# Kernel optimization log

Measured on AMD Instinct MI355X. Metric: run time of the kernel, lower is better.

Reference implementation:

```python
import jax, jax.numpy as jnp
from jax import lax
import numpy as np

B, C, PC, OC = 2, 256, 256, 256
H = W = 128
F = 2            # downsample_fac -> qkv conv kernel/stride and head upsample factor
NH, D = 4, C // 4  # 4 heads, attn_size = in_c//4
EPS = 1e-5


def conv2d(x, w, b, stride, padding):
    y = lax.conv_general_dilated(x, w, (stride, stride), padding,
                                 dimension_numbers=('NCHW', 'OIHW', 'NCHW'))
    return y + b[None, :, None, None]


def upsample_nearest(x, f):
    return jnp.repeat(jnp.repeat(x, f, axis=2), f, axis=3)


def setup_inputs() -> dict:
    key = jax.random.key(0)
    ks = jax.random.split(key, 16)
    s = 0.02  # small weight scale for numeric stability
    return {
        'app_enc':      jax.random.normal(ks[0], (B, C, H, W), jnp.float32),
        'app_pose_enc': jax.random.normal(ks[1], (B, C, H, W), jnp.float32),
        'pose_enc':     jax.random.normal(ks[2], (B, C, H, W), jnp.float32),
        'prev_inp':     jax.random.normal(ks[3], (B, PC, H // 2, W // 2), jnp.float32),
        'qw': jax.random.normal(ks[4], (NH, D, C, F, F), jnp.float32) * s,
        'qb': jax.random.normal(ks[5], (NH, D), jnp.float32) * s,
        'kw': jax.random.normal(ks[6], (NH, D, C, F, F), jnp.float32) * s,
        'kb': jax.random.normal(ks[7], (NH, D), jnp.float32) * s,
        'vw': jax.random.normal(ks[8], (NH, D, C, F, F), jnp.float32) * s,
        'vb': jax.random.normal(ks[9], (NH, D), jnp.float32) * s,
        'gamma': jax.random.normal(ks[10], (NH,), jnp.float32) * 0.1,
        'fw': jax.random.normal(ks[11], (C, 2 * C, 1, 1), jnp.float32) * s,
        'fb': jax.random.normal(ks[12], (C,), jnp.float32) * s,
        'cw': jax.random.normal(ks[13], (OC, C + PC, 3, 3), jnp.float32) * s,
        'cb': jax.random.normal(ks[14], (OC,), jnp.float32) * s,
    }


def reference(app_enc, app_pose_enc, pose_enc, prev_inp,
              qw, qb, kw, kb, vw, vb, gamma, fw, fb, cw, cb):
    # ---- AttnMech: 4 heads, q/k/v via stride-F convs over stacked heads ----
    def heads_proj(x, w, b):
        y = conv2d(x, w.reshape(NH * D, C, F, F), b.reshape(NH * D), F, 'VALID')
        _, _, h2, w2 = y.shape
        return y.reshape(B, NH, D, h2 * w2), h2, w2

    q, h2, w2 = heads_proj(pose_enc, qw, qb)        # [B,NH,D,N]
    k, _, _ = heads_proj(app_pose_enc, kw, kb)
    v, _, _ = heads_proj(app_enc, vw, vb)

    # unnormalized (no softmax) scaled dot-product attention, N = h2*w2
    attn = jnp.einsum('bhdn,bhdm->bhnm', q, k) / jnp.sqrt(jnp.float32(D))
    out = jnp.einsum('bhnm,bhdm->bhdn', attn, v)    # [B,NH,D,N]
    out = out.reshape(B, NH, D, h2, w2) * gamma[None, :, None, None, None]
    out = upsample_nearest(out.reshape(B, NH * D, h2, w2), F)  # back to [B,C,H,W]

    cat = jnp.concatenate([pose_enc, out], axis=1)  # [B, 2C, H, W]
    x = conv2d(cat, fw, fb, 1, 'VALID')             # 1x1 final_conv -> [B,C,H,W]

    # ---- GenDecAttnBlock tail: upsample prev, concat, ConvBlock ----
    prev = upsample_nearest(prev_inp, 2)            # [B,PC,H,W]
    x = jnp.concatenate([x, prev], axis=1)          # [B, C+PC, H, W]
    y = conv2d(x, cw, cb, 1, 'SAME')                # 3x3, pad 1
    mean = y.mean(axis=(2, 3), keepdims=True)
    var = y.var(axis=(2, 3), keepdims=True)         # biased, as torch InstanceNorm2d
    y = (y - mean) / jnp.sqrt(var + EPS)
    return jax.nn.relu(y)
```

## Files before the change

### kernel.cpp

```cpp
#include <hip/hip_runtime.h>
#include <hip/hip_bf16.h>

#define N2   4096
#define HWP  16384
#define EPSI 1e-5f

typedef unsigned short ushort_t;
typedef __attribute__((ext_vector_type(8))) short short8;
typedef __attribute__((ext_vector_type(4))) float f32x4;

static const size_t BUF0_OFF  = 0;
static const size_t BUF1_OFF  = 4194304;
static const size_t QT_OFF    = 8388608;
static const size_t KC_OFF    = 9437184;
static const size_t VC_OFF    = 10485760;
static const size_t S_OFF     = 11534336;
static const size_t SUM_OFF   = 11567104;
static const size_t SUM2_OFF  = 11567616;
static const size_t ZP_OFF    = 11568128;
static const size_t XCAT_OFF  = 11568192;
static const size_t PREVT_OFF = 15762496;
static const size_t WQ_OFF    = 16811072;
static const size_t WK_OFF    = 16942144;
static const size_t WV_OFF    = 17073216;
static const size_t WF_OFF    = 17204288;
static const size_t WA3X_OFF  = 17269824;
static const size_t WP_OFF    = 17564736;
static const size_t Y3_OFF    = BUF1_OFF;

__device__ __forceinline__ ushort_t f2bf(float x) {
    union { float f; unsigned u; } v; v.f = x;
    unsigned r = v.u + 0x7FFFu + ((v.u >> 16) & 1u);
    return (ushort_t)(r >> 16);
}
__device__ __forceinline__ float bf2f(ushort_t h) {
    union { unsigned u; float f; } v; v.u = ((unsigned)h) << 16; return v.f;
}
__device__ __forceinline__ void gload_lds16(const void* g, void* l) {
    __builtin_amdgcn_global_load_lds(
        (const __attribute__((address_space(1))) void*)g,
        (__attribute__((address_space(3))) void*)l, 16, 0, 0);
}

__global__ __launch_bounds__(256) void prep_k(const float* __restrict__ qw,
                                              const float* __restrict__ kw,
                                              const float* __restrict__ vw,
                                              const float* __restrict__ fw,
                                              const float* __restrict__ cw,
                                              const float* __restrict__ prev,
                                              float* __restrict__ wsf) {
    __shared__ ushort_t T[64][64];
    int sec = blockIdx.y, bx = blockIdx.x, t = threadIdx.x;
    if (sec < 3) {
        if (bx >= 256) return;
        int idx = bx * 256 + t;
        const float* src = sec == 0 ? qw : (sec == 1 ? kw : vw);
        ushort_t* dst = (ushort_t*)(wsf + (sec == 0 ? WQ_OFF : (sec == 1 ? WK_OFF : WV_OFF)));
        float4 v = *(const float4*)&src[(size_t)idx * 4];
        dst[0 * 65536 + idx] = f2bf(v.x);
        dst[1 * 65536 + idx] = f2bf(v.y);
        dst[2 * 65536 + idx] = f2bf(v.z);
        dst[3 * 65536 + idx] = f2bf(v.w);
    } else if (sec == 3) {
        int idx = bx * 256 + t;
        ((ushort_t*)(wsf + WF_OFF))[idx] = f2bf(fw[idx]);
    } else if (sec == 4) {
        int idx = bx * 256 + t;
        int oc = idx >> 9, c = idx & 511;
        const float* src = cw + (size_t)idx * 9;
        float w[9];
#pragma unroll
        for (int tp = 0; tp < 9; ++tp) w[tp] = src[tp];
        if (c < 256) {
            ushort_t* wA3x = (ushort_t*)(wsf + WA3X_OFF);
#pragma unroll
            for (int tp = 0; tp < 9; ++tp)
                wA3x[((size_t)tp * 256 + oc) * 256 + c] = f2bf(w[tp]);
        } else {
            int cc = c - 256;
            ushort_t* wP = (ushort_t*)(wsf + WP_OFF);
#pragma unroll
            for (int fx = 0; fx < 3; ++fx) {
                wP[((size_t)(0 * 6 + 0 * 3 + fx) * 256 + oc) * 256 + cc] = f2bf(w[fx]);
                wP[((size_t)(0 * 6 + 1 * 3 + fx) * 256 + oc) * 256 + cc] = f2bf(w[3 + fx] + w[6 + fx]);
                wP[((size_t)(1 * 6 + 0 * 3 + fx) * 256 + oc) * 256 + cc] = f2bf(w[fx] + w[3 + fx]);
                wP[((size_t)(1 * 6 + 1 * 3 + fx) * 256 + oc) * 256 + cc] = f2bf(w[6 + fx]);
            }
        }
    } else if (sec == 5) {
        int y2 = bx & 63, ct = (bx >> 6) & 3, b = bx >> 8;
        ushort_t* pT = (ushort_t*)(wsf + PREVT_OFF);
#pragma unroll
        for (int i = 0; i < 4; ++i) {
            int s = t + i * 256;
            int cc = s >> 4, xq = s & 15;
            float4 v = *(const float4*)&prev[(((size_t)b * 256 + ct * 64 + cc) * 64 + y2) * 64 + xq * 4];
            ushort4 h; h.x = f2bf(v.x); h.y = f2bf(v.y); h.z = f2bf(v.z); h.w = f2bf(v.w);
            *(ushort4*)&T[cc][xq * 4] = h;
        }
        __syncthreads();
#pragma unroll
        for (int i = 0; i < 2; ++i) {
            int w = t * 2 + i;
            int px = w >> 3, cbk = w & 7;
            short8 o;
#pragma unroll
            for (int j = 0; j < 8; ++j) o[j] = (short)T[cbk * 8 + j][px];
            *(short8*)&pT[((size_t)b * N2 + (size_t)y2 * 64 + px) * 256 + ct * 64 + cbk * 8] = o;
        }
    } else {
        int idx = bx * 256 + t;
        if (idx < 33856) wsf[S_OFF + idx] = 0.f;
    }
}

__device__ __forceinline__ void xpm_body(const float* __restrict__ in, ushort_t* __restrict__ xpm,
                                         int y, int ct, int b, int t) {
    __shared__ ushort_t T[64][128];
#pragma unroll
    for (int i = 0; i < 8; ++i) {
        int s = t + i * 256;
        int cc = s >> 5, xq = s & 31;
        float4 v = *(const float4*)&in[(((size_t)b * 256 + ct * 64 + cc) * 128 + y) * 128 + xq * 4];
        ushort4 h; h.x = f2bf(v.x); h.y = f2bf(v.y); h.z = f2bf(v.z); h.w = f2bf(v.w);
        *(ushort4*)&T[cc][xq * 4] = h;
    }
    __syncthreads();
#pragma unroll
    for (int i = 0; i < 4; ++i) {
        int w = t * 4 + i;
        int px = w >> 3, cbk = w & 7;
        short8 o;
#pragma unroll
        for (int j = 0; j < 8; ++j) o[j] = (short)T[cbk * 8 + j][px];
        *(short8*)&xpm[(((size_t)b * HWP) + (size_t)y * 128 + px) * 256 + ct * 64 + cbk * 8] = o;
    }
}

__global__ __launch_bounds__(256) void xpm2_k(const float* __restrict__ app,
                                              const float* __restrict__ app_pose,
                                              float* __restrict__ wsf) {
    int z = blockIdx.z, which = z >> 1, b = z & 1;
    const float* in = which == 0 ? app : app_pose;
    ushort_t* dst = (ushort_t*)(wsf + (which == 0 ? BUF0_OFF : BUF1_OFF));
    xpm_body(in, dst, blockIdx.x, blockIdx.y, b, threadIdx.x);
}

__global__ __launch_bounds__(256) void xpmP_k(const float* __restrict__ pose,
                                              float* __restrict__ wsf) {
    xpm_body(pose, (ushort_t*)(wsf + BUF0_OFF), blockIdx.x, blockIdx.y, blockIdx.z, threadIdx.x);
}

template<int MODE>
__device__ __forceinline__ void qkv_body(int nb, int oct, int b,
                                         const float* __restrict__ bias,
                                         const float* __restrict__ gamma,
                                         const ushort_t* __restrict__ wA,
                                         const ushort_t* __restrict__ xpm,
                                         ushort_t* __restrict__ outp) {
    int n0 = nb * 32, oc0 = oct * 128;
    __shared__ alignas(16) ushort_t As[2][128 * 64];
    __shared__ alignas(16) ushort_t Bs[2][32 * 64];
    int t = threadIdx.x, lane = t & 63, wv = t >> 6;
    int wm = wv >> 1, wn = wv & 1, l15 = lane & 15, lq = lane >> 4;
    f32x4 acc[4] = {};

    auto stage = [&](int chunk, int bufi) {
        int tap = chunk >> 2, c0 = (chunk & 3) << 6;
        int fy = tap >> 1, fx = tap & 1;
#pragma unroll
        for (int r = 0; r < 4; ++r) {
            int slot = t + r * 256;
            int row = slot >> 3, cbk = slot & 7;
            const ushort_t* src = wA + ((size_t)tap * 65536 + (size_t)(oc0 + row) * 256
                                        + c0 + ((cbk ^ (row & 7)) << 3));
            gload_lds16(src, (ushort_t*)As[bufi] + (((size_t)wv * 64 + r * 256) << 3));
        }
        {
            int n = t >> 3, cbk = t & 7;
            int ng = n0 + n;
            int iy = ((ng >> 6) << 1) + fy, ix = ((ng & 63) << 1) + fx;
            const ushort_t* src = xpm + (((size_t)b * HWP + (size_t)iy * 128 + ix) * 256
                                         + c0 + ((cbk ^ (n & 7)) << 3));
            gload_lds16(src, (ushort_t*)Bs[bufi] + ((size_t)wv * 64 << 3));
        }
    };

    stage(0, 0);
    __syncthreads();
    int buf = 0;
    for (int chunk = 0; chunk < 16; ++chunk) {
        short8 af[4][2], bf[2];
#pragma unroll
        for (int m = 0; m < 4; ++m) {
            int row = wm * 64 + m * 16 + l15;
#pragma unroll
            for (int ks = 0; ks < 2; ++ks)
                af[m][ks] = *(const short8*)&As[buf][row * 64 + (((ks * 4 + lq) ^ (row & 7)) << 3)];
        }
        {
            int col = wn * 16 + l15;
#pragma unroll
            for (int ks = 0; ks < 2; ++ks)
                bf[ks] = *(const short8*)&Bs[buf][col * 64 + (((ks * 4 + lq) ^ (col & 7)) << 3)];
        }
        if (chunk < 15) stage(chunk + 1, buf ^ 1);
#pragma unroll
        for (int ks = 0; ks < 2; ++ks)
#pragma unroll
            for (int m = 0; m < 4; ++m)
                acc[m] = __builtin_amdgcn_mfma_f32_16x16x32_bf16(af[m][ks], bf[ks], acc[m], 0, 0, 0);
        __syncthreads();
        buf ^= 1;
    }
#pragma unroll
    for (int m = 0; m < 4; ++m) {
        int col = wn * 16 + l15;
        int ng = n0 + col;
        int ocq = oc0 + wm * 64 + m * 16 + lq * 4;
        if (MODE == 0) {
            ushort4 o;
            float s0 = gamma[ocq >> 6] * 0.125f;
            o.x = f2bf((acc[m][0] + bias[ocq + 0]) * s0);
            o.y = f2bf((acc[m][1] + bias[ocq + 1]) * s0);
            o.z = f2bf((acc[m][2] + bias[ocq + 2]) * s0);
            o.w = f2bf((acc[m][3] + bias[ocq + 3]) * s0);
            *(ushort4*)&outp[((size_t)b * N2 + ng) * 256 + ocq] = o;
        } else {
#pragma unroll
            for (int r = 0; r < 4; ++r)
                outp[((size_t)(b * 256 + ocq + r)) * N2 + ng] = f2bf(acc[m][r] + bias[ocq + r]);
        }
    }
}

__global__ __launch_bounds__(256, 4) void kv_mfma(const float* __restrict__ kb_,
                                                  const float* __restrict__ vb_,
                                                  float* __restrict__ wsf) {
    int z = blockIdx.z, cv = z >> 1, b = z & 1;
    const ushort_t* wA  = (const ushort_t*)(wsf + (cv == 0 ? WV_OFF : WK_OFF));
    const ushort_t* xpm = (const ushort_t*)(wsf + (cv == 0 ? BUF0_OFF : BUF1_OFF));
    const float* bias   = cv == 0 ? vb_ : kb_;
    ushort_t* outp      = (ushort_t*)(wsf + (cv == 0 ? VC_OFF : KC_OFF));
    qkv_body<1>(blockIdx.x, blockIdx.y, b, bias, nullptr, wA, xpm, outp);
}

__global__ __launch_bounds__(256, 4) void q_mfma(const float* __restrict__ qb_,
                                                 const float* __restrict__ gamma,
                                                 float* __restrict__ wsf) {
    qkv_body<0>(blockIdx.x, blockIdx.y, blockIdx.z, qb_, gamma,
                (const ushort_t*)(wsf + WQ_OFF), (const ushort_t*)(wsf + BUF0_OFF),
                (ushort_t*)(wsf + QT_OFF));
}

__global__ __launch_bounds__(64) void attn_S_mfma(float* __restrict__ wsf) {
    int mc = blockIdx.x, bh = blockIdx.y;
    int b = bh >> 2, h = bh & 3;
    const ushort_t* vp = (const ushort_t*)(wsf + VC_OFF) + (size_t)(b * 256 + h * 64) * N2;
    const ushort_t* kp = (const ushort_t*)(wsf + KC_OFF) + (size_t)(b * 256 + h * 64) * N2;
    float* Sp = wsf + S_OFF + (size_t)bh * 4096;
    int lane = threadIdx.x, l15 = lane & 15, lq = lane >> 4;
    f32x4 acc[4][4] = {};
    for (int m0 = mc * 512; m0 < mc * 512 + 512; m0 += 32) {
        short8 af[4], bf[4];
#pragma unroll
        for (int mt = 0; mt < 4; ++mt)
            af[mt] = *(const short8*)&vp[(size_t)(mt * 16 + l15) * N2 + m0 + lq * 8];
#pragma unroll
        for (int nt = 0; nt < 4; ++nt)
            bf[nt] = *(const short8*)&kp[(size_t)(nt * 16 + l15) * N2 + m0 + lq * 8];
#pragma unroll
        for (int mt = 0; mt < 4; ++mt)
#pragma unroll
            for (int nt = 0; nt < 4; ++nt)
                acc[mt][nt] = __builtin_amdgcn_mfma_f32_16x16x32_bf16(
                    af[mt], bf[nt], acc[mt][nt], 0, 0, 0);
    }
#pragma unroll
    for (int mt = 0; mt < 4; ++mt)
#pragma unroll
        for (int nt = 0; nt < 4; ++nt)
#pragma unroll
            for (int r = 0; r < 4; ++r)
                atomicAdd(&Sp[(mt * 16 + lq * 4 + r) * 64 + nt * 16 + l15], acc[mt][nt][r]);
}

__global__ __launch_bounds__(256) void attn_O_mfma(float* __restrict__ wsf) {
    int nb = blockIdx.x, bh = blockIdx.y;
    int b = bh >> 2, h = bh & 3;
    const float* Sp = wsf + S_OFF + (size_t)bh * 4096;
    const ushort_t* qT = (const ushort_t*)(wsf + QT_OFF);
    ushort_t* attT = (ushort_t*)(wsf + KC_OFF);
    __shared__ ushort_t Sl[64][72];
    int t = threadIdx.x;
#pragma unroll
    for (int g = 0; g < 4; ++g) {
        int idx = t * 16 + g * 4;
        float4 v = *(const float4*)&Sp[idx];
        int row = idx >> 6, col = idx & 63;
        ushort4 o; o.x = f2bf(v.x); o.y = f2bf(v.y); o.z = f2bf(v.z); o.w = f2bf(v.w);
        *(ushort4*)&Sl[row][col] = o;
    }
    __syncthreads();
    int lane = t & 63, wv = t >> 6, l15 = lane & 15, lq = lane >> 4;
    int n_base = nb * 256 + wv * 64;
    f32x4 acc[4][4] = {};
#pragma unroll
    for (int ks = 0; ks < 2; ++ks) {
        short8 aS[4], bq[4];
#pragma unroll
        for (int mt = 0; mt < 4; ++mt)
            aS[mt] = *(const short8*)&Sl[mt * 16 + l15][ks * 32 + lq * 8];
#pragma unroll
        for (int nt = 0; nt < 4; ++nt)
            bq[nt] = *(const short8*)&qT[((size_t)b * N2 + n_base + nt * 16 + l15) * 256
                                         + h * 64 + ks * 32 + lq * 8];
#pragma unroll
        for (int mt = 0; mt < 4; ++mt)
#pragma unroll
            for (int nt = 0; nt < 4; ++nt)
                acc[mt][nt] = __builtin_amdgcn_mfma_f32_16x16x32_bf16(
                    aS[mt], bq[nt], acc[mt][nt], 0, 0, 0);
    }
#pragma unroll
    for (int mt = 0; mt < 4; ++mt)
#pragma unroll
        for (int nt = 0; nt < 4; ++nt) {
            int n = n_base + nt * 16 + l15;
            ushort4 o;
            o.x = f2bf(acc[mt][nt][0]); o.y = f2bf(acc[mt][nt][1]);
            o.z = f2bf(acc[mt][nt][2]); o.w = f2bf(acc[mt][nt][3]);
            *(ushort4*)&attT[((size_t)b * N2 + n) * 256 + h * 64 + mt * 16 + lq * 4] = o;
        }
}

__global__ __launch_bounds__(256, 3) void conv1x1_mfma(const float* __restrict__ fb,
                                                       float* __restrict__ wsf) {
    int lin = blockIdx.x;
    int swz = (lin & 7) * 128 + (lin >> 3);
    int xh = swz & 1, y = (swz >> 1) & 127, oct = (swz >> 8) & 1, b = swz >> 9;
    int oc0 = oct * 128, x0 = xh * 64;
    const ushort_t* wF   = (const ushort_t*)(wsf + WF_OFF);
    const ushort_t* xpm  = (const ushort_t*)(wsf + BUF0_OFF);
    const ushort_t* attT = (const ushort_t*)(wsf + KC_OFF);
    ushort_t* xcatT      = (ushort_t*)(wsf + XCAT_OFF);

    __shared__ alignas(16) ushort_t As[2][128 * 64];
    __shared__ alignas(16) ushort_t Bs[2][64 * 64];
    int t = threadIdx.x, lane = t & 63, wv = t >> 6;
    int wm = wv >> 1, wn = wv & 1, l15 = lane & 15, lq = lane >> 4;
    f32x4 acc[4][2] = {};

    auto stage = [&](int chunk, int bufi) {
        int c0 = chunk << 6;
#pragma unroll
        for (int r = 0; r < 4; ++r) {
            int slot = t + r * 256;
            int row = slot >> 3, cbk = slot & 7;
            const ushort_t* src = wF + ((size_t)(oc0 + row) * 512 + c0 + ((cbk ^ (row & 7)) << 3));
            gload_lds16(src, (ushort_t*)As[bufi] + (((size_t)wv * 64 + r * 256) << 3));
        }
#pragma unroll
        for (int r = 0; r < 2; ++r) {
            int slot = t + r * 256;
            int n = slot >> 3, cbk = slot & 7;
            int x = x0 + n;
            int sw = (cbk ^ (n & 7)) << 3;
            const ushort_t* src;
            if (c0 < 256)
                src = xpm + (((size_t)b * HWP + (size_t)y * 128 + x) * 256 + c0 + sw);
            else
                src = attT + (((size_t)b * N2 + (size_t)(y >> 1) * 64 + (x >> 1)) * 256
                              + (c0 - 256) + sw);
            gload_lds16(src, (ushort_t*)Bs[bufi] + (((size_t)wv * 64 + r * 256) << 3));
        }
    };

    stage(0, 0);
    __syncthreads();
    int buf = 0;
    for (int chunk = 0; chunk < 8; ++chunk) {
        short8 af[4][2], bf[2][2];
#pragma unroll
        for (int m = 0; m < 4; ++m) {
            int row = wm * 64 + m * 16 + l15;
#pragma unroll
            for (int ks = 0; ks < 2; ++ks)
                af[m][ks] = *(const short8*)&As[buf][row * 64 + (((ks * 4 + lq) ^ (row & 7)) << 3)];
        }
#pragma unroll
        for (int n = 0; n < 2; ++n) {
            int col = wn * 32 + n * 16 + l15;
#pragma unroll
            for (int ks = 0; ks < 2; ++ks)
                bf[n][ks] = *(const short8*)&Bs[buf][col * 64 + (((ks * 4 + lq) ^ (col & 7)) << 3)];
        }
        if (chunk < 7) stage(chunk + 1, buf ^ 1);
#pragma unroll
        for (int ks = 0; ks < 2; ++ks)
#pragma unroll
            for (int m = 0; m < 4; ++m)
#pragma unroll
                for (int n = 0; n < 2; ++n)
                    acc[m][n] = __builtin_amdgcn_mfma_f32_16x16x32_bf16(
                        af[m][ks], bf[n][ks], acc[m][n], 0, 0, 0);
        __syncthreads();
        buf ^= 1;
    }
#pragma unroll
    for (int m = 0; m < 4; ++m)
#pragma unroll
        for (int n = 0; n < 2; ++n) {
            int col = x0 + wn * 32 + n * 16 + l15;
            int ocq = oc0 + wm * 64 + m * 16 + lq * 4;
            ushort4 o;
            o.x = f2bf(acc[m][n][0] + fb[ocq + 0]);
            o.y = f2bf(acc[m][n][1] + fb[ocq + 1]);
            o.z = f2bf(acc[m][n][2] + fb[ocq + 2]);
            o.w = f2bf(acc[m][n][3] + fb[ocq + 3]);
            *(ushort4*)&xcatT[((size_t)b * HWP + (size_t)y * 128 + col) * 256 + ocq] = o;
        }
}

__global__ __launch_bounds__(256, 2) void conv3x3_mfma(const float* __restrict__ cb,
                                                       float* __restrict__ wsf) {
    int lin = blockIdx.x;
    int swz = (lin & 7) * 64 + (lin >> 3);
    int y = swz & 127, oct = (swz >> 7) & 1, b = swz >> 8;
    int oc0 = oct * 128;
    int py = y & 1, yh = y >> 1;

    const ushort_t* xcatT = (const ushort_t*)(wsf + XCAT_OFF);
    const ushort_t* prevT = (const ushort_t*)(wsf + PREVT_OFF);
    const ushort_t* wA3x  = (const ushort_t*)(wsf + WA3X_OFF);
    const ushort_t* wP    = (const ushort_t*)(wsf + WP_OFF);
    const ushort_t* zp    = (const ushort_t*)(wsf + ZP_OFF);
    ushort_t* y3          = (ushort_t*)(wsf + Y3_OFF);

    __shared__ alignas(16) ushort_t As[128 * 64];
    __shared__ alignas(16) ushort_t Bs[128 * 64];
    int t = threadIdx.x, lane = t & 63, wv = t >> 6;
    int wm = wv >> 1, wn = wv & 1, l15 = lane & 15, lq = lane >> 4;
    f32x4 acc[4][4] = {};

    for (int chunk = 0; chunk < 60; ++chunk) {
        if (chunk < 36) {
            int tap = chunk >> 2, c0 = (chunk & 3) << 6;
            int fy = tap / 3, fx = tap - fy * 3;
            int yy = y + fy - 1;
#pragma unroll
            for (int r = 0; r < 4; ++r) {
                int slot = t + r * 256;
                int row = slot >> 3, cbk = slot & 7;
                const ushort_t* src = wA3x + (((size_t)tap * 256 + oc0 + row) * 256
                                              + c0 + ((cbk ^ (row & 7)) << 3));
                gload_lds16(src, (ushort_t*)As + (((size_t)wv * 64 + r * 256) << 3));
            }
#pragma unroll
            for (int r = 0; r < 4; ++r) {
                int slot = t + r * 256;
                int n = slot >> 3, cbk = slot & 7;
                int xx = n + fx - 1;
                int sw = (cbk ^ (n & 7)) << 3;
                bool ok = (yy >= 0) && (yy < 128) && (xx >= 0) && (xx < 128);
                const ushort_t* src = ok
                    ? xcatT + (((size_t)b * HWP + (size_t)yy * 128 + xx) * 256 + c0 + sw)
                    : zp;
                gload_lds16(src, (ushort_t*)Bs + (((size_t)wv * 64 + r * 256) << 3));
            }
        } else {
            int pt = (chunk - 36) >> 2, c0 = ((chunk - 36) & 3) << 6;
            int j2 = pt / 3, fx = pt - j2 * 3;
            int pr = yh + py + j2 - 1;
#pragma unroll
            for (int r = 0; r < 4; ++r) {
                int slot = t + r * 256;
                int row = slot >> 3, cbk = slot & 7;
                const ushort_t* src = wP + (((size_t)(py * 6 + pt) * 256 + oc0 + row) * 256
                                            + c0 + ((cbk ^ (row & 7)) << 3));
                gload_lds16(src, (ushort_t*)As + (((size_t)wv * 64 + r * 256) << 3));
            }
#pragma unroll
            for (int r = 0; r < 4; ++r) {
                int slot = t + r * 256;
                int n = slot >> 3, cbk = slot & 7;
                int xx = n + fx - 1;
                int pc = xx >> 1;
                int sw = (cbk ^ (n & 7)) << 3;
                bool ok = (pr >= 0) && (pr < 64) && (xx >= 0) && (xx < 128);
                const ushort_t* src = ok
                    ? prevT + (((size_t)b * N2 + (size_t)pr * 64 + pc) * 256 + c0 + sw)
                    : zp;
                gload_lds16(src, (ushort_t*)Bs + (((size_t)wv * 64 + r * 256) << 3));
            }
        }
        __syncthreads();
#pragma unroll
        for (int ks = 0; ks < 2; ++ks) {
            short8 af[4], bf[4];
#pragma unroll
            for (int m = 0; m < 4; ++m) {
                int row = wm * 64 + m * 16 + l15;
                af[m] = *(const short8*)&As[row * 64 + (((ks * 4 + lq) ^ (row & 7)) << 3)];
            }
#pragma unroll
            for (int n = 0; n < 4; ++n) {
                int col = wn * 64 + n * 16 + l15;
                bf[n] = *(const short8*)&Bs[col * 64 + (((ks * 4 + lq) ^ (col & 7)) << 3)];
            }
#pragma unroll
            for (int m = 0; m < 4; ++m)
#pragma unroll
                for (int n = 0; n < 4; ++n)
                    acc[m][n] = __builtin_amdgcn_mfma_f32_16x16x32_bf16(
                        af[m], bf[n], acc[m][n], 0, 0, 0);
        }
        __syncthreads();
    }

#pragma unroll
    for (int m = 0; m < 4; ++m)
#pragma unroll
        for (int n = 0; n < 4; ++n) {
            int col = wn * 64 + n * 16 + l15;
            size_t pxo = (size_t)y * 128 + col;
#pragma unroll
            for (int r = 0; r < 4; ++r) {
                int oc = oc0 + wm * 64 + m * 16 + lq * 4 + r;
                y3[((size_t)b * 256 + oc) * HWP + pxo] = f2bf(acc[m][n][r] + cb[oc]);
            }
        }
}

__global__ __launch_bounds__(256) void inorm_relu_k(const float* __restrict__ wsf,
                                                    float* __restrict__ out) {
    int bc = blockIdx.x;
    const ushort_t* yp = (const ushort_t*)(wsf + Y3_OFF) + (size_t)bc * HWP;
    int t = threadIdx.x;
    float s1 = 0.f, s2 = 0.f;
#pragma unroll
    for (int i = 0; i < 8; ++i) {
        short8 v = *(const short8*)&yp[(size_t)(t + i * 256) * 8];
#pragma unroll
        for (int j = 0; j < 8; ++j) {
            float f = bf2f((ushort_t)v[j]);
            s1 += f; s2 += f * f;
        }
    }
#pragma unroll
    for (int o = 32; o; o >>= 1) {
        s1 += __shfl_xor(s1, o, 64);
        s2 += __shfl_xor(s2, o, 64);
    }
    __shared__ float r1[4], r2[4];
    if ((t & 63) == 0) { r1[t >> 6] = s1; r2[t >> 6] = s2; }
    __syncthreads();
    float S1 = r1[0] + r1[1] + r1[2] + r1[3];
    float S2 = r2[0] + r2[1] + r2[2] + r2[3];
    float mean = S1 * (1.f / HWP);
    float var  = S2 * (1.f / HWP) - mean * mean;
    float inv  = rsqrtf(var + EPSI);
    float* op = out + (size_t)bc * HWP;
#pragma unroll
    for (int i = 0; i < 8; ++i) {
        int base = (t + i * 256) * 8;
        short8 v = *(const short8*)&yp[(size_t)base];
        float4 o0, o1;
        o0.x = fmaxf((bf2f((ushort_t)v[0]) - mean) * inv, 0.f);
        o0.y = fmaxf((bf2f((ushort_t)v[1]) - mean) * inv, 0.f);
        o0.z = fmaxf((bf2f((ushort_t)v[2]) - mean) * inv, 0.f);
        o0.w = fmaxf((bf2f((ushort_t)v[3]) - mean) * inv, 0.f);
        o1.x = fmaxf((bf2f((ushort_t)v[4]) - mean) * inv, 0.f);
        o1.y = fmaxf((bf2f((ushort_t)v[5]) - mean) * inv, 0.f);
        o1.z = fmaxf((bf2f((ushort_t)v[6]) - mean) * inv, 0.f);
        o1.w = fmaxf((bf2f((ushort_t)v[7]) - mean) * inv, 0.f);
        *(float4*)&op[base]     = o0;
        *(float4*)&op[base + 4] = o1;
    }
}

extern "C" void kernel_launch(void* const* d_in, const int* in_sizes, int n_in,
                              void* d_out, int out_size, void* d_ws, size_t ws_size,
                              hipStream_t stream)
{
    (void)in_sizes; (void)n_in; (void)out_size; (void)ws_size;
    const float* app_enc  = (const float*)d_in[0];
    const float* app_pose = (const float*)d_in[1];
    const float* pose_enc = (const float*)d_in[2];
    const float* prev_inp = (const float*)d_in[3];
    const float* qw = (const float*)d_in[4];
    const float* qb = (const float*)d_in[5];
    const float* kw = (const float*)d_in[6];
    const float* kb = (const float*)d_in[7];
    const float* vw = (const float*)d_in[8];
    const float* vb = (const float*)d_in[9];
    const float* gamma = (const float*)d_in[10];
    const float* fw = (const float*)d_in[11];
    const float* fb = (const float*)d_in[12];
    const float* cw = (const float*)d_in[13];
    const float* cb = (const float*)d_in[14];
    float* ws  = (float*)d_ws;
    float* out = (float*)d_out;

    prep_k<<<dim3(512, 7), 256, 0, stream>>>(qw, kw, vw, fw, cw, prev_inp, ws);
    xpm2_k<<<dim3(128, 4, 4), 256, 0, stream>>>(app_enc, app_pose, ws);
    kv_mfma<<<dim3(128, 2, 4), 256, 0, stream>>>(kb, vb, ws);
    attn_S_mfma<<<dim3(8, 8), 64, 0, stream>>>(ws);
    xpmP_k<<<dim3(128, 4, 2), 256, 0, stream>>>(pose_enc, ws);
    q_mfma<<<dim3(128, 2, 2), 256, 0, stream>>>(qb, gamma, ws);
    attn_O_mfma<<<dim3(16, 8), 256, 0, stream>>>(ws);
    conv1x1_mfma<<<1024, 256, 0, stream>>>(fb, ws);
    conv3x3_mfma<<<512, 256, 0, stream>>>(cb, ws);
    inorm_relu_k<<<512, 256, 0, stream>>>(ws, out);
}
```

Baseline: 190.9 us.

## Parity-split output columns in conv3x3 to cut upsampled-prev taps; widen attn_S grid

The prev-input part of the 3x3 conv is re-expressed per output-column parity. The folded weights are precomputed for each (row parity, column parity) pair, so each output needs 2x2 low-res taps instead of 2x3. That cuts the prev K-chunks from 24 to 16 (60 to 52 chunks in total), at the cost of a doubled A tile in LDS and permuted output columns. Separately, the attn_S split-K grid is widened from 8 to 32 chunks to give more parallelism to a tiny launch, which relies on the existing accumulation of partial results.

```diff
diff --git a/kernel.cpp b/kernel.cpp
--- a/kernel.cpp
+++ b/kernel.cpp
@@ -25,7 +25,7 @@
 static const size_t WV_OFF    = 17073216;
 static const size_t WF_OFF    = 17204288;
 static const size_t WA3X_OFF  = 17269824;
-static const size_t WP_OFF    = 17564736;
+static const size_t WPP_OFF   = 17564736;
 static const size_t Y3_OFF    = BUF1_OFF;
 
 __device__ __forceinline__ ushort_t f2bf(float x) {
@@ -78,13 +78,24 @@
                 wA3x[((size_t)tp * 256 + oc) * 256 + c] = f2bf(w[tp]);
         } else {
             int cc = c - 256;
-            ushort_t* wP = (ushort_t*)(wsf + WP_OFF);
-#pragma unroll
-            for (int fx = 0; fx < 3; ++fx) {
-                wP[((size_t)(0 * 6 + 0 * 3 + fx) * 256 + oc) * 256 + cc] = f2bf(w[fx]);
-                wP[((size_t)(0 * 6 + 1 * 3 + fx) * 256 + oc) * 256 + cc] = f2bf(w[3 + fx] + w[6 + fx]);
-                wP[((size_t)(1 * 6 + 0 * 3 + fx) * 256 + oc) * 256 + cc] = f2bf(w[fx] + w[3 + fx]);
-                wP[((size_t)(1 * 6 + 1 * 3 + fx) * 256 + oc) * 256 + cc] = f2bf(w[6 + fx]);
+            ushort_t* wPP = (ushort_t*)(wsf + WPP_OFF);
+#pragma unroll
+            for (int py = 0; py < 2; ++py) {
+                float rs[2][3];
+#pragma unroll
+                for (int fx = 0; fx < 3; ++fx) {
+                    if (py == 0) { rs[0][fx] = w[fx];           rs[1][fx] = w[3 + fx] + w[6 + fx]; }
+                    else         { rs[0][fx] = w[fx] + w[3 + fx]; rs[1][fx] = w[6 + fx]; }
+                }
+#pragma unroll
+                for (int pxp = 0; pxp < 2; ++pxp)
+#pragma unroll
+                    for (int j2 = 0; j2 < 2; ++j2) {
+                        float v0 = pxp == 0 ? rs[j2][0] : rs[j2][0] + rs[j2][1];
+                        float v1 = pxp == 0 ? rs[j2][1] + rs[j2][2] : rs[j2][2];
+                        wPP[(((size_t)((py * 2 + pxp) * 4 + j2 * 2 + 0)) * 256 + oc) * 256 + cc] = f2bf(v0);
+                        wPP[(((size_t)((py * 2 + pxp) * 4 + j2 * 2 + 1)) * 256 + oc) * 256 + cc] = f2bf(v1);
+                    }
             }
         }
     } else if (sec == 5) {
@@ -261,7 +272,7 @@
     float* Sp = wsf + S_OFF + (size_t)bh * 4096;
     int lane = threadIdx.x, l15 = lane & 15, lq = lane >> 4;
     f32x4 acc[4][4] = {};
-    for (int m0 = mc * 512; m0 < mc * 512 + 512; m0 += 32) {
+    for (int m0 = mc * 128; m0 < mc * 128 + 128; m0 += 32) {
         short8 af[4], bf[4];
 #pragma unroll
         for (int mt = 0; mt < 4; ++mt)
@@ -433,18 +444,19 @@
     const ushort_t* xcatT = (const ushort_t*)(wsf + XCAT_OFF);
     const ushort_t* prevT = (const ushort_t*)(wsf + PREVT_OFF);
     const ushort_t* wA3x  = (const ushort_t*)(wsf + WA3X_OFF);
-    const ushort_t* wP    = (const ushort_t*)(wsf + WP_OFF);
+    const ushort_t* wPP   = (const ushort_t*)(wsf + WPP_OFF);
     const ushort_t* zp    = (const ushort_t*)(wsf + ZP_OFF);
     ushort_t* y3          = (ushort_t*)(wsf + Y3_OFF);
 
-    __shared__ alignas(16) ushort_t As[128 * 64];
+    __shared__ alignas(16) ushort_t As[2 * 128 * 64];
     __shared__ alignas(16) ushort_t Bs[128 * 64];
     int t = threadIdx.x, lane = t & 63, wv = t >> 6;
     int wm = wv >> 1, wn = wv & 1, l15 = lane & 15, lq = lane >> 4;
     f32x4 acc[4][4] = {};
 
-    for (int chunk = 0; chunk < 60; ++chunk) {
-        if (chunk < 36) {
+    for (int chunk = 0; chunk < 52; ++chunk) {
+        bool isPrev = chunk >= 36;
+        if (!isPrev) {
             int tap = chunk >> 2, c0 = (chunk & 3) << 6;
             int fy = tap / 3, fx = tap - fy * 3;
             int yy = y + fy - 1;
@@ -460,7 +472,8 @@
             for (int r = 0; r < 4; ++r) {
                 int slot = t + r * 256;
                 int n = slot >> 3, cbk = slot & 7;
-                int xx = n + fx - 1;
+                int x = 2 * (n & 63) + (n >> 6);
+                int xx = x + fx - 1;
                 int sw = (cbk ^ (n & 7)) << 3;
                 bool ok = (yy >= 0) && (yy < 128) && (xx >= 0) && (xx < 128);
                 const ushort_t* src = ok
@@ -469,25 +482,26 @@
                 gload_lds16(src, (ushort_t*)Bs + (((size_t)wv * 64 + r * 256) << 3));
             }
         } else {
-            int pt = (chunk - 36) >> 2, c0 = ((chunk - 36) & 3) << 6;
-            int j2 = pt / 3, fx = pt - j2 * 3;
+            int pi = chunk - 36;
+            int tap4 = pi >> 2, c0 = (pi & 3) << 6;
+            int j2 = tap4 >> 1, i2 = tap4 & 1;
             int pr = yh + py + j2 - 1;
 #pragma unroll
-            for (int r = 0; r < 4; ++r) {
+            for (int r = 0; r < 8; ++r) {
                 int slot = t + r * 256;
-                int row = slot >> 3, cbk = slot & 7;
-                const ushort_t* src = wP + (((size_t)(py * 6 + pt) * 256 + oc0 + row) * 256
-                                            + c0 + ((cbk ^ (row & 7)) << 3));
+                int p = slot >> 10, rem = slot & 1023;
+                int row = rem >> 3, cbk = rem & 7;
+                const ushort_t* src = wPP + (((size_t)((py * 2 + p) * 4 + tap4) * 256
+                                              + oc0 + row) * 256 + c0 + ((cbk ^ (row & 7)) << 3));
                 gload_lds16(src, (ushort_t*)As + (((size_t)wv * 64 + r * 256) << 3));
             }
 #pragma unroll
             for (int r = 0; r < 4; ++r) {
                 int slot = t + r * 256;
                 int n = slot >> 3, cbk = slot & 7;
-                int xx = n + fx - 1;
-                int pc = xx >> 1;
+                int pc = (n & 63) - 1 + i2 + (n >> 6);
                 int sw = (cbk ^ (n & 7)) << 3;
-                bool ok = (pr >= 0) && (pr < 64) && (xx >= 0) && (xx < 128);
+                bool ok = (pr >= 0) && (pr < 64) && (pc >= 0) && (pc < 64);
                 const ushort_t* src = ok
                     ? prevT + (((size_t)b * N2 + (size_t)pr * 64 + pc) * 256 + c0 + sw)
                     : zp;
@@ -495,13 +509,14 @@
             }
         }
         __syncthreads();
+        int abase = isPrev ? wn * 8192 : 0;
 #pragma unroll
         for (int ks = 0; ks < 2; ++ks) {
             short8 af[4], bf[4];
 #pragma unroll
             for (int m = 0; m < 4; ++m) {
                 int row = wm * 64 + m * 16 + l15;
-                af[m] = *(const short8*)&As[row * 64 + (((ks * 4 + lq) ^ (row & 7)) << 3)];
+                af[m] = *(const short8*)&As[abase + row * 64 + (((ks * 4 + lq) ^ (row & 7)) << 3)];
             }
 #pragma unroll
             for (int n = 0; n < 4; ++n) {
@@ -523,7 +538,8 @@
 #pragma unroll
         for (int n = 0; n < 4; ++n) {
             int col = wn * 64 + n * 16 + l15;
-            size_t pxo = (size_t)y * 128 + col;
+            int x = 2 * (col & 63) + (col >> 6);
+            size_t pxo = (size_t)y * 128 + x;
 #pragma unroll
             for (int r = 0; r < 4; ++r) {
                 int oc = oc0 + wm * 64 + m * 16 + lq * 4 + r;
@@ -605,7 +621,7 @@
     prep_k<<<dim3(512, 7), 256, 0, stream>>>(qw, kw, vw, fw, cw, prev_inp, ws);
     xpm2_k<<<dim3(128, 4, 4), 256, 0, stream>>>(app_enc, app_pose, ws);
     kv_mfma<<<dim3(128, 2, 4), 256, 0, stream>>>(kb, vb, ws);
-    attn_S_mfma<<<dim3(8, 8), 64, 0, stream>>>(ws);
+    attn_S_mfma<<<dim3(32, 8), 64, 0, stream>>>(ws);
     xpmP_k<<<dim3(128, 4, 2), 256, 0, stream>>>(pose_enc, ws);
     q_mfma<<<dim3(128, 2, 2), 256, 0, stream>>>(qb, gamma, ws);
     attn_O_mfma<<<dim3(16, 8), 256, 0, stream>>>(ws);
```

Measured after the change: 180.6 us. 1.06x faster.
